# Kernel optimization log

Measured on AMD Instinct MI355X. Metric: run time of the kernel, lower is better.

## Reference

```python
import jax, jax.numpy as jnp
import numpy as np

B, L, D = 8, 8192, 512   # batch, seq_len (q_len == kv_len), model dim
H, K = 8, 64             # heads, head_dim
W = 128                  # chunk width == stride (non-overlapping chunks)


def setup_inputs() -> dict:
    key = jax.random.key(0)
    ks = jax.random.split(key, 6)
    s = 1.0 / np.sqrt(D)
    return {
        "inputs_q": jax.random.normal(ks[0], (B, L, D), jnp.float32),
        "inputs_kv": jax.random.normal(ks[1], (B, L, D), jnp.float32),
        "Wq": jax.random.normal(ks[2], (D, H, K), jnp.float32) * s,
        "Wk": jax.random.normal(ks[3], (D, H, K), jnp.float32) * s,
        "Wv": jax.random.normal(ks[4], (D, H, K), jnp.float32) * s,
        "Wo": jax.random.normal(ks[5], (H, K, D), jnp.float32) * s,
    }


def reference(inputs_q, inputs_kv, Wq, Wk, Wv, Wo):
    # LocalAttentionLayer with q/kv_chunk_width == stride == W and
    # always_attend_to_first_position=True. Since width == stride the chunks
    # are non-overlapping, so the per-chunk Python loop of the original is
    # equivalent to a batched reshape into [B, C, W, ...] chunks. QKV
    # projections are position-wise, so projecting the full sequence first is
    # exactly the same math as projecting each chunk.
    C = L // W  # number of chunks
    scale = 1.0 / jnp.sqrt(jnp.asarray(K, inputs_q.dtype))

    q = jnp.einsum('bld,dhk->blhk', inputs_q, Wq) * scale  # [B,L,H,K]
    k = jnp.einsum('bld,dhk->blhk', inputs_kv, Wk)
    v = jnp.einsum('bld,dhk->blhk', inputs_kv, Wv)

    qc = q.reshape(B, C, W, H, K)
    kc = k.reshape(B, C, W, H, K)
    vc = v.reshape(B, C, W, H, K)

    # Global first KV position ([CLS]) prepended to every chunk's keys/values,
    # matching `kv_cls = inputs_kv[..., 0:1, :]; concat([kv_cls, chunk])`.
    k_cls = jnp.broadcast_to(k[:, None, 0:1], (B, C, 1, H, K))
    v_cls = jnp.broadcast_to(v[:, None, 0:1], (B, C, 1, H, K))
    kc = jnp.concatenate([k_cls, kc], axis=2)  # [B,C,W+1,H,K]
    vc = jnp.concatenate([v_cls, vc], axis=2)

    scores = jnp.einsum('bcqhk,bcmhk->bchqm', qc, kc)  # [B,C,H,W,W+1]
    attn = jax.nn.softmax(scores, axis=-1)
    ctx = jnp.einsum('bchqm,bcmhk->bcqhk', attn, vc)   # [B,C,W,H,K]
    ctx = ctx.reshape(B, L, H, K)
    return jnp.einsum('blhk,hkd->bld', ctx, Wo)        # [B,L,D]
```

## Files before the change

### kernel.cpp

```cpp
#include <hip/hip_runtime.h>
#include <hip/hip_bf16.h>
#include <type_traits>

#define B_ 8
#define L_ 8192
#define D_ 512
#define H_ 8
#define KD_ 64
#define W_ 128
#define C_ 64
#define M_ (B_ * L_)
#define HK_ 512

typedef __bf16 bf16_t;
typedef __bf16 bf16x8 __attribute__((ext_vector_type(8)));
typedef float f32x4 __attribute__((ext_vector_type(4)));

#define GLOAD16(gp, lp)                                                        \
  __builtin_amdgcn_global_load_lds(                                            \
      (const __attribute__((address_space(1))) unsigned int*)(gp),             \
      (__attribute__((address_space(3))) unsigned int*)(lp), 16, 0, 0)

__global__ void prep_weights_kernel(const float* __restrict__ Wq,
                                    const float* __restrict__ Wk,
                                    const float* __restrict__ Wv,
                                    const float* __restrict__ Wo,
                                    bf16_t* __restrict__ wt) {
  const int n = blockIdx.x;
  const int mat = blockIdx.y;
  const float* src = (mat == 0) ? Wq : (mat == 1) ? Wk : (mat == 2) ? Wv : Wo;
  const float scale = (mat == 0) ? 0.125f : 1.0f;
  bf16_t* dst = wt + ((size_t)mat * 512 + n) * 512;
  for (int d = threadIdx.x; d < 512; d += blockDim.x) {
    dst[d] = (bf16_t)(src[(size_t)d * 512 + n] * scale);
  }
}

__global__ void cvt_x_kernel(const float* __restrict__ xq,
                             const float* __restrict__ xkv,
                             bf16_t* __restrict__ oq,
                             bf16_t* __restrict__ okv) {
  const float* src = blockIdx.y ? xkv : xq;
  bf16_t* dst = blockIdx.y ? okv : oq;
  const size_t e = ((size_t)blockIdx.x * blockDim.x + threadIdx.x) * 8;
  float4 a = *reinterpret_cast<const float4*>(src + e);
  float4 b = *reinterpret_cast<const float4*>(src + e + 4);
  bf16x8 o;
  o[0] = (bf16_t)a.x; o[1] = (bf16_t)a.y; o[2] = (bf16_t)a.z; o[3] = (bf16_t)a.w;
  o[4] = (bf16_t)b.x; o[5] = (bf16_t)b.y; o[6] = (bf16_t)b.z; o[7] = (bf16_t)b.w;
  *reinterpret_cast<bf16x8*>(dst + e) = o;
}

template <typename OT>
__global__ __launch_bounds__(256, 2)
void gemm_bt16(const bf16_t* __restrict__ A, const bf16_t* __restrict__ BT,
               OT* __restrict__ Cmat, OT* __restrict__ C2, int Ndim) {
  __shared__ bf16_t sA[128 * 64];
  __shared__ bf16_t sB[128 * 64];

  const int tid = threadIdx.x;
  const int lane = tid & 63;
  const int w = tid >> 6;
  const int wr = (w >> 1) * 64;
  const int wc = (w & 1) * 64;
  const int m0 = blockIdx.y * 128;
  const int n0 = blockIdx.x * 128;

  const bool second = (n0 >= Ndim);
  OT* const outp = second ? C2 : Cmat;
  const int n0o = second ? (n0 - Ndim) : n0;

  const int srow = tid >> 3;
  const int scol = (tid & 7) * 8;
  const int cl = lane & 15;
  const int g = lane >> 4;
  const int Kdim = 512;

  f32x4 acc[4][4] = {};

  for (int k0 = 0; k0 < Kdim; k0 += 64) {
#pragma unroll
    for (int i = 0; i < 4; i++) {
      const bf16_t* gp = A + (size_t)(m0 + i * 32 + srow) * Kdim + k0 + scol;
      char* lp = (char*)sA + i * 4096 + w * 1024;
      GLOAD16(gp, lp);
    }
#pragma unroll
    for (int i = 0; i < 4; i++) {
      const bf16_t* gp = BT + (size_t)(n0 + i * 32 + srow) * Kdim + k0 + scol;
      char* lp = (char*)sB + i * 4096 + w * 1024;
      GLOAD16(gp, lp);
    }
    __syncthreads();

#pragma unroll
    for (int kk = 0; kk < 2; kk++) {
      bf16x8 afr[4], bfr[4];
#pragma unroll
      for (int t = 0; t < 4; t++)
        afr[t] = *reinterpret_cast<const bf16x8*>(
            &sA[(wr + t * 16 + cl) * 64 + kk * 32 + g * 8]);
#pragma unroll
      for (int t = 0; t < 4; t++)
        bfr[t] = *reinterpret_cast<const bf16x8*>(
            &sB[(wc + t * 16 + cl) * 64 + kk * 32 + g * 8]);
#pragma unroll
      for (int i = 0; i < 4; i++)
#pragma unroll
        for (int j = 0; j < 4; j++)
          acc[i][j] = __builtin_amdgcn_mfma_f32_16x16x32_bf16(afr[i], bfr[j],
                                                              acc[i][j], 0, 0, 0);
    }
    __syncthreads();
  }

  const int crow = (lane >> 4) * 4;
  const int ccol = lane & 15;
#pragma unroll
  for (int i = 0; i < 4; i++) {
#pragma unroll
    for (int j = 0; j < 4; j++) {
      const int gm = m0 + wr + i * 16 + crow;
      const int gn = n0o + wc + j * 16 + ccol;
#pragma unroll
      for (int jj = 0; jj < 4; jj++) {
        const float vv = acc[i][j][jj];
        if constexpr (std::is_same<OT, float>::value)
          outp[(size_t)(gm + jj) * Ndim + gn] = vv;
        else
          outp[(size_t)(gm + jj) * Ndim + gn] = (bf16_t)vv;
      }
    }
  }
}

__global__ __launch_bounds__(256, 2)
void attn_kernel(const bf16_t* __restrict__ q, const bf16_t* __restrict__ k,
                 const bf16_t* __restrict__ v, bf16_t* __restrict__ ctx) {
  const int h = blockIdx.x;
  const int c = blockIdx.y;
  const int b = blockIdx.z;
  const int tid = threadIdx.x;
  const int lane = tid & 63;
  const int w = tid >> 6;
  const int cl = lane & 15;
  const int g = lane >> 4;

  __shared__ bf16_t vT[64][136];
  __shared__ bf16_t pL[128][136];
  __shared__ float scls[128];
  __shared__ float pclsn[128];
  __shared__ float kcls[64];
  __shared__ float vcls[64];

  const size_t headoff = (size_t)h * KD_;
  const size_t rowbase = (size_t)b * L_ + (size_t)c * W_;

  if (tid < 64) {
    kcls[tid] = (float)k[(size_t)b * L_ * HK_ + headoff + tid];
    vcls[tid] = (float)v[(size_t)b * L_ * HK_ + headoff + tid];
  }
  {
    const int m = tid >> 1;
    const int kd0 = (tid & 1) * 32;
    const bf16_t* vp = v + (rowbase + m) * HK_ + headoff + kd0;
#pragma unroll
    for (int i = 0; i < 4; i++) {
      bf16x8 t8 = *reinterpret_cast<const bf16x8*>(vp + i * 8);
#pragma unroll
      for (int j = 0; j < 8; j++) vT[kd0 + i * 8 + j][m] = t8[j];
    }
  }

  bf16x8 qf[2][2];
#pragma unroll
  for (int rt = 0; rt < 2; rt++)
#pragma unroll
    for (int kk = 0; kk < 2; kk++) {
      const size_t row = rowbase + w * 32 + rt * 16 + cl;
      qf[rt][kk] = *reinterpret_cast<const bf16x8*>(&q[row * HK_ + headoff + kk * 32 + g * 8]);
    }

  f32x4 sacc[2][8] = {};
#pragma unroll
  for (int ct = 0; ct < 8; ct++) {
    bf16x8 kf[2];
#pragma unroll
    for (int kk = 0; kk < 2; kk++) {
      const size_t rowm = rowbase + ct * 16 + cl;
      kf[kk] = *reinterpret_cast<const bf16x8*>(&k[rowm * HK_ + headoff + kk * 32 + g * 8]);
    }
#pragma unroll
    for (int rt = 0; rt < 2; rt++)
#pragma unroll
      for (int kk = 0; kk < 2; kk++)
        sacc[rt][ct] = __builtin_amdgcn_mfma_f32_16x16x32_bf16(qf[rt][kk], kf[kk], sacc[rt][ct], 0, 0, 0);
  }

  __syncthreads();

#pragma unroll
  for (int rt = 0; rt < 2; rt++) {
    float part = 0.f;
#pragma unroll
    for (int kk = 0; kk < 2; kk++)
#pragma unroll
      for (int j = 0; j < 8; j++)
        part += (float)qf[rt][kk][j] * kcls[kk * 32 + g * 8 + j];
    part += __shfl_xor(part, 16);
    part += __shfl_xor(part, 32);
    if (g == 0) scls[w * 32 + rt * 16 + cl] = part;
  }

  float invd[2][4];
#pragma unroll
  for (int rt = 0; rt < 2; rt++) {
#pragma unroll
    for (int jj = 0; jj < 4; jj++) {
      float mx = sacc[rt][0][jj];
#pragma unroll
      for (int ct = 1; ct < 8; ct++) mx = fmaxf(mx, sacc[rt][ct][jj]);
#pragma unroll
      for (int d = 1; d < 16; d <<= 1) mx = fmaxf(mx, __shfl_xor(mx, d));
      const float sc = scls[w * 32 + rt * 16 + g * 4 + jj];
      mx = fmaxf(mx, sc);
      float sum = 0.f;
#pragma unroll
      for (int ct = 0; ct < 8; ct++) {
        const float e = __expf(sacc[rt][ct][jj] - mx);
        sacc[rt][ct][jj] = e;
        sum += e;
      }
#pragma unroll
      for (int d = 1; d < 16; d <<= 1) sum += __shfl_xor(sum, d);
      const float pc = __expf(sc - mx);
      sum += pc;
      const float inv = 1.0f / sum;
      invd[rt][jj] = inv;
      if (cl == 0) pclsn[w * 32 + rt * 16 + g * 4 + jj] = pc * inv;
    }
  }

#pragma unroll
  for (int rt = 0; rt < 2; rt++)
#pragma unroll
    for (int jj = 0; jj < 4; jj++) {
      const int row = w * 32 + rt * 16 + g * 4 + jj;
#pragma unroll
      for (int ct = 0; ct < 8; ct++)
        pL[row][ct * 16 + cl] = (bf16_t)(sacc[rt][ct][jj] * invd[rt][jj]);
    }
  __syncthreads();

  f32x4 cacc[2][4] = {};
#pragma unroll
  for (int kk = 0; kk < 4; kk++) {
    bf16x8 vf[4];
#pragma unroll
    for (int c2 = 0; c2 < 4; c2++)
      vf[c2] = *reinterpret_cast<const bf16x8*>(&vT[c2 * 16 + cl][kk * 32 + g * 8]);
#pragma unroll
    for (int rt = 0; rt < 2; rt++) {
      const bf16x8 pf = *reinterpret_cast<const bf16x8*>(&pL[w * 32 + rt * 16 + cl][kk * 32 + g * 8]);
#pragma unroll
      for (int c2 = 0; c2 < 4; c2++)
        cacc[rt][c2] = __builtin_amdgcn_mfma_f32_16x16x32_bf16(pf, vf[c2], cacc[rt][c2], 0, 0, 0);
    }
  }

#pragma unroll
  for (int rt = 0; rt < 2; rt++)
#pragma unroll
    for (int c2 = 0; c2 < 4; c2++)
#pragma unroll
      for (int jj = 0; jj < 4; jj++) {
        const int row = w * 32 + rt * 16 + g * 4 + jj;
        const int kd = c2 * 16 + cl;
        const float val = cacc[rt][c2][jj] + pclsn[row] * vcls[kd];
        ctx[(rowbase + row) * HK_ + headoff + kd] = (bf16_t)val;
      }
}

extern "C" void kernel_launch(void* const* d_in, const int* in_sizes, int n_in,
                              void* d_out, int out_size, void* d_ws, size_t ws_size,
                              hipStream_t stream) {
  const float* Xq = (const float*)d_in[0];
  const float* Xkv = (const float*)d_in[1];
  const float* Wq = (const float*)d_in[2];
  const float* Wk = (const float*)d_in[3];
  const float* Wv = (const float*)d_in[4];
  const float* Wo = (const float*)d_in[5];
  float* out = (float*)d_out;

  char* ws = (char*)d_ws;
  bf16_t* wT = (bf16_t*)ws;
  size_t off = (size_t)4 * 512 * 512 * sizeof(bf16_t);
  bf16_t* xqb  = (bf16_t*)(ws + off); off += (size_t)M_ * D_ * 2;
  bf16_t* xkvb = (bf16_t*)(ws + off); off += (size_t)M_ * D_ * 2;
  bf16_t* qb = (bf16_t*)(ws + off); off += (size_t)M_ * HK_ * 2;
  bf16_t* kb = (bf16_t*)(ws + off); off += (size_t)M_ * HK_ * 2;
  bf16_t* vb = (bf16_t*)(ws + off);
  bf16_t* ctxb = xqb;

  bf16_t* wTq = wT;
  bf16_t* wTk = wT + (size_t)512 * 512;
  bf16_t* wTo = wT + (size_t)3 * 512 * 512;

  prep_weights_kernel<<<dim3(512, 4), 128, 0, stream>>>(Wq, Wk, Wv, Wo, wT);
  cvt_x_kernel<<<dim3(M_ * D_ / 8 / 256, 2), 256, 0, stream>>>(Xq, Xkv, xqb, xkvb);

  gemm_bt16<bf16_t><<<dim3(4, M_ / 128), 256, 0, stream>>>(xqb, wTq, qb, qb, HK_);
  gemm_bt16<bf16_t><<<dim3(8, M_ / 128), 256, 0, stream>>>(xkvb, wTk, kb, vb, HK_);

  attn_kernel<<<dim3(H_, C_, B_), 256, 0, stream>>>(qb, kb, vb, ctxb);

  gemm_bt16<float><<<dim3(4, M_ / 128), 256, 0, stream>>>(ctxb, wTo, out, out, D_);
}
```

Before: 422.0 us.

## Merge Q and KV projections into one GEMM launch with XCD-aware block swizzling

```diff
diff --git a/kernel.cpp b/kernel.cpp
--- a/kernel.cpp
+++ b/kernel.cpp
@@ -51,24 +51,33 @@
   *reinterpret_cast<bf16x8*>(dst + e) = o;
 }
 
-template <typename OT>
-__global__ __launch_bounds__(256, 2)
-void gemm_bt16(const bf16_t* __restrict__ A, const bf16_t* __restrict__ BT,
-               OT* __restrict__ Cmat, OT* __restrict__ C2, int Ndim) {
+template <typename OT, int NX>
+__global__ __launch_bounds__(256, 3)
+void gemm_bt16(const bf16_t* __restrict__ A0, const bf16_t* __restrict__ A1,
+               const bf16_t* __restrict__ BT,
+               OT* __restrict__ C0, OT* __restrict__ C1, OT* __restrict__ C2) {
   __shared__ bf16_t sA[128 * 64];
   __shared__ bf16_t sB[128 * 64];
+
+  const int nb = gridDim.x;
+  const int chunk = nb >> 3;
+  const int bid = blockIdx.x;
+  const int swz = (bid & 7) * chunk + (bid >> 3);
+  const int my = swz / NX;
+  const int mx = swz - my * NX;
+  const int m0 = my * 128;
+  const int seg = mx >> 2;
+  const int n0o = (mx & 3) * 128;
+  const int nB0 = mx * 128;
+
+  const bf16_t* const A = (seg == 0) ? A0 : A1;
+  OT* const outp = (seg == 0) ? C0 : (seg == 1) ? C1 : C2;
 
   const int tid = threadIdx.x;
   const int lane = tid & 63;
   const int w = tid >> 6;
   const int wr = (w >> 1) * 64;
   const int wc = (w & 1) * 64;
-  const int m0 = blockIdx.y * 128;
-  const int n0 = blockIdx.x * 128;
-
-  const bool second = (n0 >= Ndim);
-  OT* const outp = second ? C2 : Cmat;
-  const int n0o = second ? (n0 - Ndim) : n0;
 
   const int srow = tid >> 3;
   const int scol = (tid & 7) * 8;
@@ -87,7 +96,7 @@
     }
 #pragma unroll
     for (int i = 0; i < 4; i++) {
-      const bf16_t* gp = BT + (size_t)(n0 + i * 32 + srow) * Kdim + k0 + scol;
+      const bf16_t* gp = BT + (size_t)(nB0 + i * 32 + srow) * Kdim + k0 + scol;
       char* lp = (char*)sB + i * 4096 + w * 1024;
       GLOAD16(gp, lp);
     }
@@ -126,20 +135,24 @@
       for (int jj = 0; jj < 4; jj++) {
         const float vv = acc[i][j][jj];
         if constexpr (std::is_same<OT, float>::value)
-          outp[(size_t)(gm + jj) * Ndim + gn] = vv;
+          outp[(size_t)(gm + jj) * 512 + gn] = vv;
         else
-          outp[(size_t)(gm + jj) * Ndim + gn] = (bf16_t)vv;
+          outp[(size_t)(gm + jj) * 512 + gn] = (bf16_t)vv;
       }
     }
   }
 }
 
-__global__ __launch_bounds__(256, 2)
+__global__ __launch_bounds__(256, 3)
 void attn_kernel(const bf16_t* __restrict__ q, const bf16_t* __restrict__ k,
                  const bf16_t* __restrict__ v, bf16_t* __restrict__ ctx) {
-  const int h = blockIdx.x;
-  const int c = blockIdx.y;
-  const int b = blockIdx.z;
+  const int bid = blockIdx.x;
+  const int swz = (bid & 7) * 512 + (bid >> 3);
+  const int h = swz & 7;
+  const int cb = swz >> 3;
+  const int c = cb & 63;
+  const int b = cb >> 6;
+
   const int tid = threadIdx.x;
   const int lane = tid & 63;
   const int w = tid >> 6;
@@ -148,17 +161,16 @@
 
   __shared__ bf16_t vT[64][136];
   __shared__ bf16_t pL[128][136];
-  __shared__ float scls[128];
-  __shared__ float pclsn[128];
-  __shared__ float kcls[64];
-  __shared__ float vcls[64];
+  __shared__ float scl[128];
+  __shared__ bf16_t kcls[64];
+  __shared__ bf16_t vcls[64];
 
   const size_t headoff = (size_t)h * KD_;
   const size_t rowbase = (size_t)b * L_ + (size_t)c * W_;
 
   if (tid < 64) {
-    kcls[tid] = (float)k[(size_t)b * L_ * HK_ + headoff + tid];
-    vcls[tid] = (float)v[(size_t)b * L_ * HK_ + headoff + tid];
+    kcls[tid] = k[(size_t)b * L_ * HK_ + headoff + tid];
+    vcls[tid] = v[(size_t)b * L_ * HK_ + headoff + tid];
   }
   {
     const int m = tid >> 1;
@@ -206,10 +218,10 @@
     for (int kk = 0; kk < 2; kk++)
 #pragma unroll
       for (int j = 0; j < 8; j++)
-        part += (float)qf[rt][kk][j] * kcls[kk * 32 + g * 8 + j];
+        part += (float)qf[rt][kk][j] * (float)kcls[kk * 32 + g * 8 + j];
     part += __shfl_xor(part, 16);
     part += __shfl_xor(part, 32);
-    if (g == 0) scls[w * 32 + rt * 16 + cl] = part;
+    if (g == 0) scl[w * 32 + rt * 16 + cl] = part;
   }
 
   float invd[2][4];
@@ -222,7 +234,7 @@
       for (int ct = 1; ct < 8; ct++) mx = fmaxf(mx, sacc[rt][ct][jj]);
 #pragma unroll
       for (int d = 1; d < 16; d <<= 1) mx = fmaxf(mx, __shfl_xor(mx, d));
-      const float sc = scls[w * 32 + rt * 16 + g * 4 + jj];
+      const float sc = scl[w * 32 + rt * 16 + g * 4 + jj];
       mx = fmaxf(mx, sc);
       float sum = 0.f;
 #pragma unroll
@@ -237,7 +249,7 @@
       sum += pc;
       const float inv = 1.0f / sum;
       invd[rt][jj] = inv;
-      if (cl == 0) pclsn[w * 32 + rt * 16 + g * 4 + jj] = pc * inv;
+      if (cl == 0) scl[w * 32 + rt * 16 + g * 4 + jj] = pc * inv;
     }
   }
 
@@ -276,7 +288,7 @@
       for (int jj = 0; jj < 4; jj++) {
         const int row = w * 32 + rt * 16 + g * 4 + jj;
         const int kd = c2 * 16 + cl;
-        const float val = cacc[rt][c2][jj] + pclsn[row] * vcls[kd];
+        const float val = cacc[rt][c2][jj] + scl[row] * (float)vcls[kd];
         ctx[(rowbase + row) * HK_ + headoff + kd] = (bf16_t)val;
       }
 }
@@ -302,17 +314,17 @@
   bf16_t* vb = (bf16_t*)(ws + off);
   bf16_t* ctxb = xqb;
 
-  bf16_t* wTq = wT;
-  bf16_t* wTk = wT + (size_t)512 * 512;
+  bf16_t* wTqkv = wT;
   bf16_t* wTo = wT + (size_t)3 * 512 * 512;
 
   prep_weights_kernel<<<dim3(512, 4), 128, 0, stream>>>(Wq, Wk, Wv, Wo, wT);
   cvt_x_kernel<<<dim3(M_ * D_ / 8 / 256, 2), 256, 0, stream>>>(Xq, Xkv, xqb, xkvb);
 
-  gemm_bt16<bf16_t><<<dim3(4, M_ / 128), 256, 0, stream>>>(xqb, wTq, qb, qb, HK_);
-  gemm_bt16<bf16_t><<<dim3(8, M_ / 128), 256, 0, stream>>>(xkvb, wTk, kb, vb, HK_);
-
-  attn_kernel<<<dim3(H_, C_, B_), 256, 0, stream>>>(qb, kb, vb, ctxb);
-
-  gemm_bt16<float><<<dim3(4, M_ / 128), 256, 0, stream>>>(ctxb, wTo, out, out, D_);
-}
+  gemm_bt16<bf16_t, 12><<<dim3(12 * (M_ / 128)), 256, 0, stream>>>(
+      xqb, xkvb, wTqkv, qb, kb, vb);
+
+  attn_kernel<<<dim3(H_ * C_ * B_), 256, 0, stream>>>(qb, kb, vb, ctxb);
+
+  gemm_bt16<float, 4><<<dim3(4 * (M_ / 128)), 256, 0, stream>>>(
+      ctxb, ctxb, wTo, out, out, out);
+}
```

Measured after the change: 386.9 us. 1.09x faster.
